# Performance work log

Hardware: AMD Instinct MI355X
Metric: run time of the kernel (lower is better)

Reference implementation:

```python
import jax, jax.numpy as jnp
import numpy as np

B, S, D, H = 4, 2048, 1024, 16
HD = D // H  # head size = 64

def setup_inputs() -> dict:
    key = jax.random.key(0)
    ks = jax.random.split(key, 9)
    s = 1.0 / np.sqrt(D)
    inp = {"x": jax.random.normal(ks[0], (B, S, D), dtype=jnp.float32)}
    for i, n in enumerate(["q", "k", "v", "o"]):
        inp[f"W{n}"] = jax.random.uniform(ks[1 + 2 * i], (D, D), minval=-s, maxval=s, dtype=jnp.float32)
        inp[f"b{n}"] = jax.random.uniform(ks[2 + 2 * i], (D,), minval=-s, maxval=s, dtype=jnp.float32)
    return inp

def reference(x, Wq, bq, Wk, bk, Wv, bv, Wo, bo):
    b, s, d = x.shape
    # project and split heads: [b, h, s, hd]
    def heads(y):
        return y.reshape(b, s, H, HD).transpose(0, 2, 1, 3)
    q = heads(x @ Wq.T + bq)
    k = heads(x @ Wk.T + bk)
    v = heads(x @ Wv.T + bv)
    scores = jnp.einsum('bhqd,bhkd->bhqk', q, k) / jnp.sqrt(jnp.float32(HD))
    attn = jax.nn.softmax(scores, axis=-1)
    ctx = jnp.einsum('bhqk,bhkd->bhqd', attn, v)
    ctx = ctx.transpose(0, 2, 1, 3).reshape(b, s, d)
    return ctx @ Wo.T + bo
```

## Files before the change

### kernel.cpp

```cpp
#include <hip/hip_runtime.h>
#include <hip/hip_bf16.h>

typedef __bf16 bf16;
typedef __bf16 bf16x8 __attribute__((ext_vector_type(8)));
typedef __bf16 bf16x4 __attribute__((ext_vector_type(4)));
typedef float f32x4 __attribute__((ext_vector_type(4)));
typedef float f32x16 __attribute__((ext_vector_type(16)));
typedef unsigned int u32;
typedef u32 u32x4 __attribute__((ext_vector_type(4)));

#define B_ 4
#define S_ 2048
#define D_ 1024
#define H_ 16
#define HD_ 64
#define LOG2E 1.4426950408889634f

static __device__ __forceinline__ f32x4 mfma16(bf16x8 a, bf16x8 b, f32x4 c) {
  return __builtin_amdgcn_mfma_f32_16x16x32_bf16(a, b, c, 0, 0, 0);
}
static __device__ __forceinline__ f32x16 mfma32(bf16x8 a, bf16x8 b, f32x16 c) {
  return __builtin_amdgcn_mfma_f32_32x32x16_bf16(a, b, c, 0, 0, 0);
}
static __device__ __forceinline__ void gload_lds16(const void* g, void* l) {
  __builtin_amdgcn_global_load_lds(
      (const __attribute__((address_space(1))) void*)g,
      (__attribute__((address_space(3))) void*)l, 16, 0, 0);
}
static __device__ __forceinline__ u32 pack2(float lo, float hi) {
  union { bf16 h[2]; u32 u; } un;
  un.h[0] = (bf16)lo; un.h[1] = (bf16)hi;
  return un.u;
}

__global__ void cvt_kernel(const float* __restrict__ in, bf16* __restrict__ out, int n4) {
  int i = blockIdx.x * blockDim.x + threadIdx.x;
  const int stride = gridDim.x * blockDim.x;
  for (; i < n4; i += stride) {
    float4 v = reinterpret_cast<const float4*>(in)[i];
    bf16x4 o;
    o[0] = (bf16)v.x; o[1] = (bf16)v.y; o[2] = (bf16)v.z; o[3] = (bf16)v.w;
    reinterpret_cast<bf16x4*>(out)[i] = o;
  }
}
__global__ void cvtw_kernel(const float* __restrict__ w0, const float* __restrict__ w1,
                            const float* __restrict__ w2, const float* __restrict__ w3,
                            bf16* __restrict__ o0, bf16* __restrict__ o1,
                            bf16* __restrict__ o2, bf16* __restrict__ o3, int n4) {
  const float* in = blockIdx.y == 0 ? w0 : blockIdx.y == 1 ? w1 : blockIdx.y == 2 ? w2 : w3;
  bf16* out = blockIdx.y == 0 ? o0 : blockIdx.y == 1 ? o1 : blockIdx.y == 2 ? o2 : o3;
  const int i = blockIdx.x * blockDim.x + threadIdx.x;
  float4 v = reinterpret_cast<const float4*>(in)[i];
  bf16x4 o;
  o[0] = (bf16)v.x; o[1] = (bf16)v.y; o[2] = (bf16)v.z; o[3] = (bf16)v.w;
  reinterpret_cast<bf16x4*>(out)[i] = o;
}

template<bool OUT_BF16, bool BIAS_ROW>
__global__ __launch_bounds__(256, 2)
void gemm3(const bf16* __restrict__ A, const bf16* __restrict__ W,
           const float* __restrict__ bias, void* __restrict__ Cout,
           int M, int N, int K, float scale) {
  __shared__ __align__(16) char lds[73728];
  const int tid = threadIdx.x;
  const int wave = tid >> 6;
  const int lane = tid & 63;
  const int g = lane >> 4, r16 = lane & 15;
  const unsigned nwgx = gridDim.x;
  const unsigned nwg = nwgx * gridDim.y;
  unsigned lid = blockIdx.x + nwgx * blockIdx.y;
  unsigned swz = (lid & 7) * (nwg >> 3) + (lid >> 3);
  const int m0 = (int)(swz / nwgx) * 128, n0 = (int)(swz % nwgx) * 256;
  const int wm = (wave >> 1) * 64, wn = (wave & 1) * 128;

  f32x4 acc[4][8] = {};

  const int arow0 = tid >> 2;
  const int acol = ((tid & 3) ^ ((tid >> 3) & 3)) * 8;
  const int wdst = wave * 1024;
  const int nkt = K >> 5;

  auto stage = [&](int bi, int t) {
    char* buf = lds + bi * 24576;
    const int kb = t << 5;
#pragma unroll
    for (int q = 0; q < 2; ++q)
      gload_lds16(&A[(size_t)(m0 + q * 64 + arow0) * K + kb + acol],
                  buf + q * 4096 + wdst);
#pragma unroll
    for (int q = 0; q < 4; ++q)
      gload_lds16(&W[(size_t)(n0 + q * 64 + arow0) * K + kb + acol],
                  buf + 8192 + q * 4096 + wdst);
  };

  stage(0, 0);
  stage(1, 1);
  int cur = 0;

  for (int t = 0; t < nkt; ++t) {
    if (t + 1 < nkt) asm volatile("s_waitcnt vmcnt(6)" ::: "memory");
    else             asm volatile("s_waitcnt vmcnt(0)" ::: "memory");
    __builtin_amdgcn_s_barrier();
    int nx2 = cur + 2; if (nx2 >= 3) nx2 -= 3;
    if (t + 2 < nkt) stage(nx2, t + 2);

    const char* bufA = lds + cur * 24576;
    const char* bufB = bufA + 8192;
    bf16x8 af[4], bfr[8];
#pragma unroll
    for (int i = 0; i < 4; ++i) {
      const int ra = wm + i * 16 + r16;
      af[i] = *reinterpret_cast<const bf16x8*>(
          bufA + ra * 64 + ((g ^ ((ra >> 1) & 3)) << 4));
    }
#pragma unroll
    for (int j = 0; j < 8; ++j) {
      const int rb = wn + j * 16 + r16;
      bfr[j] = *reinterpret_cast<const bf16x8*>(
          bufB + rb * 64 + ((g ^ ((rb >> 1) & 3)) << 4));
    }
    __builtin_amdgcn_s_setprio(1);
#pragma unroll
    for (int i = 0; i < 4; ++i)
#pragma unroll
      for (int j = 0; j < 8; ++j)
        acc[i][j] = mfma16(af[i], bfr[j], acc[i][j]);
    __builtin_amdgcn_s_setprio(0);
    cur = (cur + 1 == 3) ? 0 : cur + 1;
  }

#pragma unroll
  for (int i = 0; i < 4; ++i) {
#pragma unroll
    for (int j = 0; j < 8; ++j) {
      const int col = n0 + wn + j * 16 + r16;
      float bcol = BIAS_ROW ? 0.f : bias[col];
#pragma unroll
      for (int r = 0; r < 4; ++r) {
        const int row = m0 + wm + i * 16 + g * 4 + r;
        const float bv = BIAS_ROW ? bias[row] : bcol;
        const float v = (acc[i][j][r] + bv) * scale;
        if (OUT_BF16)
          reinterpret_cast<bf16*>(Cout)[(size_t)row * N + col] = (bf16)v;
        else
          reinterpret_cast<float*>(Cout)[(size_t)row * N + col] = v;
      }
    }
  }
}

#define VMB(N) do { asm volatile("s_waitcnt vmcnt(" #N ")" ::: "memory"); \
                    __builtin_amdgcn_s_barrier(); } while (0)

__global__ __launch_bounds__(256, 2)
void attn_kernel(const bf16* __restrict__ Q, const bf16* __restrict__ K,
                 const bf16* __restrict__ Vt, bf16* __restrict__ CTX) {
  const unsigned nwg = gridDim.x * gridDim.y;
  const unsigned lid = blockIdx.x + gridDim.x * blockIdx.y;
  const unsigned swzid = (lid & 7) * (nwg >> 3) + (lid >> 3);
  const int bh = (int)(swzid >> 3);
  const int q0 = (int)(swzid & 7) * 256;
  const int h = bh & (H_ - 1), b = bh >> 4;
  const int tid = threadIdx.x, wave = tid >> 6, lane = tid & 63;
  const int l32 = lane & 31, hi = lane >> 5;

  const bf16* Qb  = Q  + ((size_t)b * S_) * D_ + h * HD_;
  const bf16* Kb  = K  + ((size_t)b * S_) * D_ + h * HD_;
  const bf16* Vtb = Vt + (size_t)(h * HD_) * (B_ * S_) + b * S_;

  __shared__ __align__(16) char lds[49152];
  char* const kb0 = lds;             char* const vb0 = lds + 24576;
  char* const kb1 = lds + 8192;      char* const vb1 = lds + 32768;
  char* const kb2 = lds + 16384;     char* const vb2 = lds + 40960;

  const int qbase = q0 + wave * 64;
  bf16x8 qf0[4], qf1[4];
#pragma unroll
  for (int ks = 0; ks < 4; ++ks) {
    qf0[ks] = *reinterpret_cast<const bf16x8*>(&Qb[(size_t)(qbase + l32) * D_ + ks * 16 + hi * 8]);
    qf1[ks] = *reinterpret_cast<const bf16x8*>(&Qb[(size_t)(qbase + 32 + l32) * D_ + ks * 16 + hi * 8]);
  }

  bf16x8 onesf;
#pragma unroll
  for (int j = 0; j < 8; ++j) onesf[j] = (bf16)1.0f;

  f32x16 ctx00 = {}, ctx01 = {}, ctx10 = {}, ctx11 = {};
  f32x16 lacc0 = {}, lacc1 = {};

  const int krow0 = wave * 16 + (lane >> 3);
  const int xs = ((lane & 7) ^ (lane >> 3)) * 8;
  const int stoff = wave * 2048;
  const int swl = (l32 & 7) << 4;
  int coa[4];
#pragma unroll
  for (int ks = 0; ks < 4; ++ks) coa[ks] = (ks * 32 + hi * 16) ^ swl;
  const int rA = l32 * 128, rB = (32 + l32) * 128;

  const bf16* Kst = Kb  + (size_t)krow0 * D_ + xs;
  const bf16* Vst = Vtb + (size_t)krow0 * (B_ * S_) + xs;

  auto stage = [&](char* kd, char* vd) {
    gload_lds16(Kst,                  kd + stoff);
    gload_lds16(Kst + 8 * D_,         kd + stoff + 1024);
    gload_lds16(Vst,                  vd + stoff);
    gload_lds16(Vst + 8 * (B_ * S_),  vd + stoff + 1024);
    Kst += 64 * D_;
    Vst += 64;
  };

  auto expack = [&](const f32x16& s, u32* w) {
#pragma unroll
    for (int a = 0; a < 4; ++a)
#pragma unroll
      for (int c = 0; c < 2; ++c)
        w[2 * a + c] = pack2(__builtin_amdgcn_exp2f(s[4 * a + 2 * c]),
                             __builtin_amdgcn_exp2f(s[4 * a + 2 * c + 1]));
  };

  auto compute = [&](const char* bK, const char* bV) {
    bf16x8 kf0[4], kf1[4];
#pragma unroll
    for (int ks = 0; ks < 4; ++ks) {
      kf0[ks] = *reinterpret_cast<const bf16x8*>(bK + rA + coa[ks]);
      kf1[ks] = *reinterpret_cast<const bf16x8*>(bK + rB + coa[ks]);
    }
    const f32x16 z = {};
    f32x16 s00, s01;
    __builtin_amdgcn_s_setprio(1);
    s00 = mfma32(kf0[0], qf0[0], z);
    s01 = mfma32(kf1[0], qf0[0], z);
#pragma unroll
    for (int ks = 1; ks < 4; ++ks) {
      s00 = mfma32(kf0[ks], qf0[ks], s00);
      s01 = mfma32(kf1[ks], qf0[ks], s01);
    }
    __builtin_amdgcn_s_setprio(0);
    u32 w00[8], w01[8];
    expack(s00, w00); expack(s01, w01);
    f32x16 s10, s11;
    __builtin_amdgcn_s_setprio(1);
    s10 = mfma32(kf0[0], qf1[0], z);
    s11 = mfma32(kf1[0], qf1[0], z);
#pragma unroll
    for (int ks = 1; ks < 4; ++ks) {
      s10 = mfma32(kf0[ks], qf1[ks], s10);
      s11 = mfma32(kf1[ks], qf1[ks], s11);
    }
    __builtin_amdgcn_s_setprio(0);
    u32 w10[8], w11[8];
    expack(s10, w10); expack(s11, w11);
    bf16x8 vf0[4], vf1[4];
#pragma unroll
    for (int ksp = 0; ksp < 4; ++ksp) {
      vf0[ksp] = *reinterpret_cast<const bf16x8*>(bV + rA + coa[ksp]);
      vf1[ksp] = *reinterpret_cast<const bf16x8*>(bV + rB + coa[ksp]);
    }
#pragma unroll
    for (int m = 0; m < 2; ++m) {
      const u32* wlo = m ? w10 : w00;
      const u32* whi = m ? w11 : w01;
      f32x16& la = m ? lacc1 : lacc0;
      f32x16& c0 = m ? ctx10 : ctx00;
      f32x16& c1 = m ? ctx11 : ctx01;
#pragma unroll
      for (int T = 0; T < 2; ++T) {
        const u32* w = T ? whi : wlo;
#pragma unroll
        for (int k1 = 0; k1 < 2; ++k1) {
          auto rAp = __builtin_amdgcn_permlane32_swap((int)w[4 * k1 + 0], (int)w[4 * k1 + 2], false, false);
          auto rBp = __builtin_amdgcn_permlane32_swap((int)w[4 * k1 + 1], (int)w[4 * k1 + 3], false, false);
          u32x4 fw;
          fw[0] = (u32)rAp[0]; fw[1] = (u32)rBp[0]; fw[2] = (u32)rAp[1]; fw[3] = (u32)rBp[1];
          const bf16x8 pa = __builtin_bit_cast(bf16x8, fw);
          const int ksp = 2 * T + k1;
          __builtin_amdgcn_s_setprio(1);
          la = mfma32(pa, onesf, la);
          c0 = mfma32(pa, vf0[ksp], c0);
          c1 = mfma32(pa, vf1[ksp], c1);
          __builtin_amdgcn_s_setprio(0);
        }
      }
    }
  };

  stage(kb0, vb0);
  stage(kb1, vb1);

  for (int u = 0; u < 10; ++u) {
    VMB(4); stage(kb2, vb2); compute(kb0, vb0);
    VMB(4); stage(kb0, vb0); compute(kb1, vb1);
    VMB(4); stage(kb1, vb1); compute(kb2, vb2);
  }
  VMB(4); compute(kb0, vb0);
  VMB(0); compute(kb1, vb1);
  __syncthreads();

  char* Cw = lds + wave * 8192;
#pragma unroll
  for (int rg = 0; rg < 16; ++rg) {
    const int ql = (rg & 3) + 8 * (rg >> 2) + 4 * hi;
    const int swq = (ql & 7) << 4;
    {
      const float inv = 1.0f / lacc0[rg];
      *reinterpret_cast<bf16*>(Cw + ql * 128 + ((l32 * 2) ^ swq)) = (bf16)(ctx00[rg] * inv);
      *reinterpret_cast<bf16*>(Cw + ql * 128 + ((64 + l32 * 2) ^ swq)) = (bf16)(ctx01[rg] * inv);
    }
    {
      const float inv = 1.0f / lacc1[rg];
      *reinterpret_cast<bf16*>(Cw + (32 + ql) * 128 + ((l32 * 2) ^ swq)) = (bf16)(ctx10[rg] * inv);
      *reinterpret_cast<bf16*>(Cw + (32 + ql) * 128 + ((64 + l32 * 2) ^ swq)) = (bf16)(ctx11[rg] * inv);
    }
  }
  asm volatile("" ::: "memory");
#pragma unroll
  for (int i = 0; i < 8; ++i) {
    const int s = i * 64 + lane;
    const int row = s >> 3, cs = (s & 7) * 16;
    bf16x8 v = *reinterpret_cast<const bf16x8*>(Cw + row * 128 + (cs ^ ((row & 7) << 4)));
    *reinterpret_cast<bf16x8*>(
        &CTX[(size_t)(b * S_ + q0 + wave * 64 + row) * D_ + h * HD_ + cs / 2]) = v;
  }
}

extern "C" void kernel_launch(void* const* d_in, const int* in_sizes, int n_in,
                              void* d_out, int out_size, void* d_ws, size_t ws_size,
                              hipStream_t stream) {
  const float* x  = (const float*)d_in[0];
  const float* Wq = (const float*)d_in[1]; const float* bq = (const float*)d_in[2];
  const float* Wk = (const float*)d_in[3]; const float* bk = (const float*)d_in[4];
  const float* Wv = (const float*)d_in[5]; const float* bv = (const float*)d_in[6];
  const float* Wo = (const float*)d_in[7]; const float* bo = (const float*)d_in[8];

  char* ws = (char*)d_ws;
  const size_t MB = 1048576;
  bf16* xb  = (bf16*)(ws);
  bf16* wqb = (bf16*)(ws + 16 * MB);
  bf16* wkb = (bf16*)(ws + 18 * MB);
  bf16* wvb = (bf16*)(ws + 20 * MB);
  bf16* wob = (bf16*)(ws + 22 * MB);
  bf16* qb  = (bf16*)(ws + 24 * MB);
  bf16* kb  = (bf16*)(ws + 40 * MB);
  bf16* vtb = (bf16*)(ws + 56 * MB);
  bf16* ctx = (bf16*)(ws + 72 * MB);

  cvt_kernel<<<2048, 256, 0, stream>>>(x, xb, 2097152);
  cvtw_kernel<<<dim3(1024, 4), 256, 0, stream>>>(Wq, Wk, Wv, Wo, wqb, wkb, wvb, wob, 262144);

  dim3 gq(1024 / 256, 8192 / 128);
  gemm3<true,  false><<<gq, 256, 0, stream>>>(xb, wqb, bq, qb, 8192, 1024, 1024, 0.125f * LOG2E);
  gemm3<true,  false><<<gq, 256, 0, stream>>>(xb, wkb, bk, kb, 8192, 1024, 1024, 1.0f);
  dim3 gv(8192 / 256, 1024 / 128);
  gemm3<true,  true ><<<gv, 256, 0, stream>>>(wvb, xb, bv, vtb, 1024, 8192, 1024, 1.0f);

  attn_kernel<<<dim3(8, 64), 256, 0, stream>>>(qb, kb, vtb, ctx);

  gemm3<false, false><<<gq, 256, 0, stream>>>(ctx, wob, bo, d_out, 8192, 1024, 1024, 1.0f);
}
```

Before: 195.6 us.

## Fuse Q and K projections into one GEMM with interleaved QK output

```diff
diff --git a/kernel.cpp b/kernel.cpp
--- a/kernel.cpp
+++ b/kernel.cpp
@@ -14,6 +14,7 @@
 #define D_ 1024
 #define H_ 16
 #define HD_ 64
+#define QKLD 2048
 #define LOG2E 1.4426950408889634f
 
 static __device__ __forceinline__ f32x4 mfma16(bf16x8 a, bf16x8 b, f32x4 c) {
@@ -149,12 +150,96 @@
   }
 }
 
+__global__ __launch_bounds__(256, 2)
+void gemm_qk(const bf16* __restrict__ A, const bf16* __restrict__ W,
+             const float* __restrict__ bq, const float* __restrict__ bk,
+             bf16* __restrict__ Cout) {
+  __shared__ __align__(16) char lds[49152];
+  const int tid = threadIdx.x;
+  const int wave = tid >> 6;
+  const int lane = tid & 63;
+  const int g = lane >> 4, r16 = lane & 15;
+  const int K = 1024;
+  const unsigned nwgx = gridDim.x;
+  const unsigned nwg = nwgx * gridDim.y;
+  unsigned lid = blockIdx.x + nwgx * blockIdx.y;
+  unsigned swz = (lid & 7) * (nwg >> 3) + (lid >> 3);
+  const int m0 = (int)(swz / nwgx) * 128, n0 = (int)(swz % nwgx) * 128;
+  const int wm = (wave >> 1) * 64, wn = (wave & 1) * 64;
+
+  f32x4 acc[4][4] = {};
+
+  const int nkt = K >> 5;
+
+  auto stage = [&](int bi, int t) {
+    char* buf = lds + bi * 16384;
+    const int kb = t << 5;
+#pragma unroll
+    for (int l = 0; l < 2; ++l) {
+      const int s = tid + l * 256;
+      const int row = s >> 2;
+      const int col = ((s & 3) ^ ((s >> 3) & 3)) * 8;
+      gload_lds16(&A[(size_t)(m0 + row) * K + kb + col], buf + wave * 1024 + l * 4096);
+      gload_lds16(&W[(size_t)(n0 + row) * K + kb + col], buf + 8192 + wave * 1024 + l * 4096);
+    }
+  };
+
+  stage(0, 0);
+  stage(1, 1);
+  int cur = 0;
+
+  for (int t = 0; t < nkt; ++t) {
+    if (t + 1 < nkt) asm volatile("s_waitcnt vmcnt(4)" ::: "memory");
+    else             asm volatile("s_waitcnt vmcnt(0)" ::: "memory");
+    __builtin_amdgcn_s_barrier();
+    int nx2 = cur + 2; if (nx2 >= 3) nx2 -= 3;
+    if (t + 2 < nkt) stage(nx2, t + 2);
+
+    const char* bufA = lds + cur * 16384;
+    const char* bufB = bufA + 8192;
+    bf16x8 af[4], bfr[4];
+#pragma unroll
+    for (int i = 0; i < 4; ++i) {
+      const int ra = wm + i * 16 + r16;
+      af[i] = *reinterpret_cast<const bf16x8*>(
+          bufA + ra * 64 + ((g ^ ((ra >> 1) & 3)) << 4));
+      const int rb = wn + i * 16 + r16;
+      bfr[i] = *reinterpret_cast<const bf16x8*>(
+          bufB + rb * 64 + ((g ^ ((rb >> 1) & 3)) << 4));
+    }
+    __builtin_amdgcn_s_setprio(1);
+#pragma unroll
+    for (int i = 0; i < 4; ++i)
+#pragma unroll
+      for (int j = 0; j < 4; ++j)
+        acc[i][j] = mfma16(af[i], bfr[j], acc[i][j]);
+    __builtin_amdgcn_s_setprio(0);
+    cur = (cur + 1 == 3) ? 0 : cur + 1;
+  }
+
+#pragma unroll
+  for (int i = 0; i < 4; ++i) {
+#pragma unroll
+    for (int j = 0; j < 4; ++j) {
+      const int col = n0 + wn + j * 16 + r16;
+      const bool isQ = col < 1024;
+      const float bv = isQ ? bq[col] : bk[col - 1024];
+      const float sc = isQ ? 0.125f * LOG2E : 1.0f;
+#pragma unroll
+      for (int r = 0; r < 4; ++r) {
+        const int row = m0 + wm + i * 16 + g * 4 + r;
+        Cout[(size_t)row * QKLD + col] = (bf16)((acc[i][j][r] + bv) * sc);
+      }
+    }
+  }
+}
+
 #define VMB(N) do { asm volatile("s_waitcnt vmcnt(" #N ")" ::: "memory"); \
                     __builtin_amdgcn_s_barrier(); } while (0)
 
 __global__ __launch_bounds__(256, 2)
-void attn_kernel(const bf16* __restrict__ Q, const bf16* __restrict__ K,
-                 const bf16* __restrict__ Vt, bf16* __restrict__ CTX) {
+void attn_kernel(const bf16* __restrict__ QK, const bf16* __restrict__ Vt,
+                 bf16* __restrict__ CTX) {
   const unsigned nwg = gridDim.x * gridDim.y;
   const unsigned lid = blockIdx.x + gridDim.x * blockIdx.y;
   const unsigned swzid = (lid & 7) * (nwg >> 3) + (lid >> 3);
@@ -164,8 +249,8 @@
   const int tid = threadIdx.x, wave = tid >> 6, lane = tid & 63;
   const int l32 = lane & 31, hi = lane >> 5;
 
-  const bf16* Qb  = Q  + ((size_t)b * S_) * D_ + h * HD_;
-  const bf16* Kb  = K  + ((size_t)b * S_) * D_ + h * HD_;
+  const bf16* Qb  = QK + ((size_t)b * S_) * QKLD + h * HD_;
+  const bf16* Kb  = QK + ((size_t)b * S_) * QKLD + 1024 + h * HD_;
   const bf16* Vtb = Vt + (size_t)(h * HD_) * (B_ * S_) + b * S_;
 
   __shared__ __align__(16) char lds[49152];
@@ -177,8 +262,8 @@
   bf16x8 qf0[4], qf1[4];
 #pragma unroll
   for (int ks = 0; ks < 4; ++ks) {
-    qf0[ks] = *reinterpret_cast<const bf16x8*>(&Qb[(size_t)(qbase + l32) * D_ + ks * 16 + hi * 8]);
-    qf1[ks] = *reinterpret_cast<const bf16x8*>(&Qb[(size_t)(qbase + 32 + l32) * D_ + ks * 16 + hi * 8]);
+    qf0[ks] = *reinterpret_cast<const bf16x8*>(&Qb[(size_t)(qbase + l32) * QKLD + ks * 16 + hi * 8]);
+    qf1[ks] = *reinterpret_cast<const bf16x8*>(&Qb[(size_t)(qbase + 32 + l32) * QKLD + ks * 16 + hi * 8]);
   }
 
   bf16x8 onesf;
@@ -197,15 +282,15 @@
   for (int ks = 0; ks < 4; ++ks) coa[ks] = (ks * 32 + hi * 16) ^ swl;
   const int rA = l32 * 128, rB = (32 + l32) * 128;
 
-  const bf16* Kst = Kb  + (size_t)krow0 * D_ + xs;
+  const bf16* Kst = Kb  + (size_t)krow0 * QKLD + xs;
   const bf16* Vst = Vtb + (size_t)krow0 * (B_ * S_) + xs;
 
   auto stage = [&](char* kd, char* vd) {
     gload_lds16(Kst,                  kd + stoff);
-    gload_lds16(Kst + 8 * D_,         kd + stoff + 1024);
+    gload_lds16(Kst + 8 * QKLD,       kd + stoff + 1024);
     gload_lds16(Vst,                  vd + stoff);
     gload_lds16(Vst + 8 * (B_ * S_),  vd + stoff + 1024);
-    Kst += 64 * D_;
+    Kst += 64 * QKLD;
     Vst += 64;
   };
 
@@ -339,21 +424,19 @@
   bf16* wkb = (bf16*)(ws + 18 * MB);
   bf16* wvb = (bf16*)(ws + 20 * MB);
   bf16* wob = (bf16*)(ws + 22 * MB);
-  bf16* qb  = (bf16*)(ws + 24 * MB);
-  bf16* kb  = (bf16*)(ws + 40 * MB);
+  bf16* qkb = (bf16*)(ws + 24 * MB);
   bf16* vtb = (bf16*)(ws + 56 * MB);
   bf16* ctx = (bf16*)(ws + 72 * MB);
 
   cvt_kernel<<<2048, 256, 0, stream>>>(x, xb, 2097152);
   cvtw_kernel<<<dim3(1024, 4), 256, 0, stream>>>(Wq, Wk, Wv, Wo, wqb, wkb, wvb, wob, 262144);
 
+  gemm_qk<<<dim3(16, 64), 256, 0, stream>>>(xb, wqb, bq, bk, qkb);
+  dim3 gv(8192 / 256, 1024 / 128);
+  gemm3<true, true><<<gv, 256, 0, stream>>>(wvb, xb, bv, vtb, 1024, 8192, 1024, 1.0f);
+
+  attn_kernel<<<dim3(8, 64), 256, 0, stream>>>(qkb, vtb, ctx);
+
   dim3 gq(1024 / 256, 8192 / 128);
-  gemm3<true,  false><<<gq, 256, 0, stream>>>(xb, wqb, bq, qb, 8192, 1024, 1024, 0.125f * LOG2E);
-  gemm3<true,  false><<<gq, 256, 0, stream>>>(xb, wkb, bk, kb, 8192, 1024, 1024, 1.0f);
-  dim3 gv(8192 / 256, 1024 / 128);
-  gemm3<true,  true ><<<gv, 256, 0, stream>>>(wvb, xb, bv, vtb, 1024, 8192, 1024, 1.0f);
-
-  attn_kernel<<<dim3(8, 64), 256, 0, stream>>>(qb, kb, vtb, ctx);
-
   gemm3<false, false><<<gq, 256, 0, stream>>>(ctx, wob, bo, d_out, 8192, 1024, 1024, 1.0f);
 }
```

Result: faster. 188.6 us (-3.6%).
